# Kernel tuning notes

Hardware: AMD Instinct MI355X
Metric: run time of the kernel (lower is better)

## Reference

```python
import jax, jax.numpy as jnp
import numpy as np

WS = 2        # window size
HEADS = 8
BLOCK = 4     # shuffle block
SCALE = HEADS ** (-0.5)


def conv2d(x, w, groups=1, pad=0):
    return jax.lax.conv_general_dilated(
        x, w, window_strides=(1, 1), padding=[(pad, pad), (pad, pad)],
        dimension_numbers=("NCHW", "OIHW", "NCHW"), feature_group_count=groups)


def shuffle_data(x, block):
    B, C, h, w = x.shape
    x = jnp.transpose(x, (0, 2, 3, 1)).reshape(B, h * w, C)          # b (h w) c
    x = x.reshape(B, block, h // block, block, w // block, C)
    x = jnp.transpose(x, (0, 2, 4, 1, 3, 5)).reshape(B, h * w, C)
    return jnp.transpose(x.reshape(B, h, w, C), (0, 3, 1, 2))         # b c h w


def shuffle_back(x, block):
    B, C, h, w = x.shape
    x = jnp.transpose(x, (0, 2, 3, 1)).reshape(B, h * w, C)
    x = x.reshape(B, h // block, w // block, block, block, C)
    x = jnp.transpose(x, (0, 3, 1, 4, 2, 5)).reshape(B, h * w, C)
    return jnp.transpose(x.reshape(B, h, w, C), (0, 3, 1, 2))


def msa(x):
    # x: [B, C, H, W] with C = 3*dim. NOTE: the original uses a raw reshape
    # (not a permute) to [B, H, W, C]; we replicate that exactly.
    B, C, H, W = x.shape
    x = x.reshape(B, H, W, C)
    hg, wg = H // WS, W // WS
    x = x.reshape(B, hg, WS, wg, WS, C)
    x = jnp.swapaxes(x, 2, 3)                                         # [B,hg,wg,ws,ws,C]
    head_dim = C // 3 // HEADS
    qkv = x.reshape(B, hg * wg, WS * WS, 3, HEADS, head_dim)
    qkv = jnp.transpose(qkv, (3, 0, 1, 4, 2, 5))                      # [3,B,G,h,ws*ws,d]
    q, k, v = qkv[0], qkv[1], qkv[2]
    attn = jnp.einsum("bghqd,bghkd->bghqk", q, k) * SCALE
    attn = jax.nn.softmax(attn, axis=-1)
    out = jnp.einsum("bghqk,bghkd->bghqd", attn, v)
    out = jnp.swapaxes(out, 2, 3).reshape(B, hg, wg, WS, WS, C // 3)
    out = jnp.swapaxes(out, 2, 3)                                     # [B,hg,ws,wg,ws,C/3]
    # raw reshape back to NCHW layout, matching torch .reshape semantics
    return out.reshape(B, C // 3, hg * WS, wg * WS)


def setup_inputs() -> dict:
    key = jax.random.key(0)
    k1, k2, k3, k4 = jax.random.split(key, 4)
    B, dim, H, W = 4, 192, 256, 256
    x = jax.random.normal(k1, (B, dim, H, W), dtype=jnp.float32)
    w_qkv = jax.random.normal(k2, (3 * dim, dim, 1, 1), dtype=jnp.float32) * 0.05
    w_dw = jax.random.normal(k3, (3 * dim, 1, 3, 3), dtype=jnp.float32) * 0.1
    w_proj = jax.random.normal(k4, (dim, dim, 1, 1), dtype=jnp.float32) * 0.05
    return {"x": x, "w_qkv": w_qkv, "w_dw": w_dw, "w_proj": w_proj, "shuffle": 1}


def reference(x, w_qkv, w_dw, w_proj, shuffle):
    if shuffle:
        x = shuffle_data(x, BLOCK)
    qkv = conv2d(conv2d(x, w_qkv), w_dw, groups=w_dw.shape[0], pad=1)
    attn = msa(qkv)
    out = conv2d(attn, w_proj)
    if shuffle:
        out = shuffle_back(out, BLOCK)
    return out
```

## Files before the change

### kernel.cpp

```cpp
#include <hip/hip_runtime.h>
#include <hip/hip_bf16.h>

typedef unsigned short u16;
typedef unsigned int   u32;
typedef __attribute__((ext_vector_type(8))) short s16x8;
typedef __attribute__((ext_vector_type(4))) float f32x4;

__device__ __forceinline__ u16 f2bf(float f) {
  u32 u = __builtin_bit_cast(u32, f);
  return (u16)((u + 0x7FFFu + ((u >> 16) & 1u)) >> 16);
}
__device__ __forceinline__ float bf2f(u16 h) {
  return __builtin_bit_cast(float, (u32)h << 16);
}
__device__ __forceinline__ u32 pack2(float a, float b) {
  __hip_bfloat162 h = __float22bfloat162_rn(make_float2(a, b));
  u32 r;
  __builtin_memcpy(&r, &h, 4);
  return r;
}

__global__ __launch_bounds__(256) void k_wcvt(const float* __restrict__ wq,
                                              const float* __restrict__ wp,
                                              u16* __restrict__ wq_bf,
                                              u16* __restrict__ wp_bf) {
  int i = blockIdx.x * 256 + threadIdx.x;
  if (i < 576 * 192) wq_bf[i] = f2bf(wq[i]);
  if (i < 192 * 192) wp_bf[i] = f2bf(wp[i]);
}

__global__ __launch_bounds__(768, 3) void k_qkv(const float* __restrict__ x,
                                                const u16* __restrict__ wq,
                                                u16* __restrict__ qkv1) {
  __shared__ __align__(16) u16 Xs[256 * 200];
  const int t  = threadIdx.x;
  const int b  = blockIdx.y;
  const int h1 = blockIdx.x;
  const float* xb = x + (size_t)b * 12582912;
  const int hbase = h1 >> 2;
  const int wbase = (h1 & 3) << 4;
#pragma unroll
  for (int it = 0; it < 8; ++it) {
    const int idx = it * 768 + t;
    const int f = idx & 3;
    const int r = (idx >> 2) & 15;
    const int c = (idx >> 6) * 2;
    const int ho = ((r >> 2) & 3) * 64 + hbase;
    const int wo = (r & 3) * 64 + wbase + f * 4;
    const float* s0 = xb + (size_t)c * 65536 + (size_t)ho * 256 + wo;
    float4 v0 = *(const float4*)s0;
    float4 v1 = *(const float4*)(s0 + 65536);
    const int nb = 64 * f + r;
    const int slot = c >> 3;
    const int sl = (slot & 24) | ((slot + 2 * (r & 7)) & 7);
    const int ccol = sl * 8 + (c & 7);
    *(u32*)&Xs[(nb     ) * 200 + ccol] = pack2(v0.x, v1.x);
    *(u32*)&Xs[(nb + 16) * 200 + ccol] = pack2(v0.y, v1.y);
    *(u32*)&Xs[(nb + 32) * 200 + ccol] = pack2(v0.z, v1.z);
    *(u32*)&Xs[(nb + 48) * 200 + ccol] = pack2(v0.w, v1.w);
  }
  __syncthreads();
  const int lane = t & 63, wv = t >> 6;
  const int lm = lane & 15, lk = lane >> 4;
  s16x8 wf[3][6];
#pragma unroll
  for (int mf = 0; mf < 3; ++mf) {
#pragma unroll
    for (int kk = 0; kk < 6; ++kk)
      wf[mf][kk] = *(const s16x8*)&wq[(size_t)(wv * 48 + mf * 16 + lm) * 192 + kk * 32 + lk * 8];
  }
  u16* const ob = qkv1 + (size_t)b * 37748736 + h1 * 256 + lk * 4;
  int slr[6];
#pragma unroll
  for (int kk = 0; kk < 6; ++kk) {
    const int slot = 4 * kk + lk;
    slr[kk] = ((slot & 24) | ((slot + 2 * (lm & 7)) & 7)) * 8;
  }

#pragma unroll 2
  for (int g = 0; g < 16; ++g) {
    s16x8 av[6];
#pragma unroll
    for (int kk = 0; kk < 6; ++kk)
      av[kk] = *(const s16x8*)&Xs[(g * 16 + lm) * 200 + slr[kk]];
    f32x4 acc[3];
#pragma unroll
    for (int mf = 0; mf < 3; ++mf) acc[mf] = f32x4{0.f, 0.f, 0.f, 0.f};
#pragma unroll
    for (int kk = 0; kk < 6; ++kk) {
#pragma unroll
      for (int mf = 0; mf < 3; ++mf)
        acc[mf] = __builtin_amdgcn_mfma_f32_16x16x32_bf16(av[kk], wf[mf][kk], acc[mf], 0, 0, 0);
    }
#pragma unroll
    for (int mf = 0; mf < 3; ++mf) {
      const int ch = wv * 48 + mf * 16 + lm;
      uint2 o;
      o.x = pack2(acc[mf][0], acc[mf][1]);
      o.y = pack2(acc[mf][2], acc[mf][3]);
      *(uint2*)(ob + (size_t)ch * 65536 + g * 16) = o;
    }
  }
}

__global__ __launch_bounds__(512, 2) void k_dwmsa(const u16* __restrict__ qkv1,
                                                  const float* __restrict__ wdw,
                                                  u16* __restrict__ attnb) {
  __shared__ __align__(16) u16 Ds[2][18432];
  const int t = threadIdx.x;
  const int b = blockIdx.y;
  const int gh = blockIdx.x >> 3;
  const int c0 = (blockIdx.x & 7) * 32;
  const u16* qb = qkv1 + (size_t)b * 37748736;

  {
    const int s1 = t >> 8;
    const int tl = t & 255;
    const int lane = t & 63;
    const u32 F = 576u * (u32)((2 * gh + s1) * 256 + c0);
    const int ch0 = (int)(F >> 16);
    const int ch1 = (ch0 < 575) ? ch0 + 1 : 575;
    float wa[9], wb[9];
#pragma unroll
    for (int i = 0; i < 9; ++i) { wa[i] = wdw[ch0 * 9 + i]; wb[i] = wdw[ch1 * 9 + i]; }
#pragma unroll 3
    for (int k = 0; k < 9; ++k) {
      const int ii = (tl + 256 * k) * 8;
      const u32 f = F + (u32)ii;
      const int ch = (int)(f >> 16);
      const int px = (int)(f & 65535u);
      const int h = px >> 8, w0 = px & 255;
      const u16* in = qb + ((size_t)ch << 16);
      const int hm = (h > 0) ? h - 1 : 0;
      const int hp = (h < 255) ? h + 1 : 255;
      uint4 m0 = *(const uint4*)(in + (size_t)hm * 256 + w0);
      uint4 m1 = *(const uint4*)(in + (size_t)h  * 256 + w0);
      uint4 m2 = *(const uint4*)(in + (size_t)hp * 256 + w0);
      u32 p0 = (u32)__shfl((int)m0.w, lane - 1);
      u32 p1 = (u32)__shfl((int)m1.w, lane - 1);
      u32 p2 = (u32)__shfl((int)m2.w, lane - 1);
      u32 n0 = (u32)__shfl((int)m0.x, lane + 1);
      u32 n1 = (u32)__shfl((int)m1.x, lane + 1);
      u32 n2 = (u32)__shfl((int)m2.x, lane + 1);
      const float vm = (h > 0)   ? 1.f : 0.f;
      const float vp = (h < 255) ? 1.f : 0.f;
      const float lmask = (w0 > 0) ? 1.f : 0.f;
      const float rmask = (w0 < 248) ? 1.f : 0.f;
      const bool sec = (ch != ch0);
      float w9[9];
#pragma unroll
      for (int i = 0; i < 9; ++i) w9[i] = sec ? wb[i] : wa[i];
      w9[0] *= vm; w9[1] *= vm; w9[2] *= vm;
      w9[6] *= vp; w9[7] *= vp; w9[8] *= vp;
      float acc[8] = {0.f,0.f,0.f,0.f,0.f,0.f,0.f,0.f};
      const uint4 mids[3] = {m0, m1, m2};
      const u32 prevs[3] = {p0, p1, p2};
      const u32 nexts[3] = {n0, n1, n2};
#pragma unroll
      for (int ky = 0; ky < 3; ++ky) {
        float e[10];
        e[0] = bf2f((u16)(prevs[ky] >> 16)) * lmask;
        u32 uu[4] = {mids[ky].x, mids[ky].y, mids[ky].z, mids[ky].w};
#pragma unroll
        for (int q = 0; q < 4; ++q) {
          e[1 + 2 * q] = bf2f((u16)(uu[q] & 0xffffu));
          e[2 + 2 * q] = bf2f((u16)(uu[q] >> 16));
        }
        e[9] = bf2f((u16)(nexts[ky] & 0xffffu)) * rmask;
#pragma unroll
        for (int kx = 0; kx < 3; ++kx) {
          const float wk = w9[ky * 3 + kx];
#pragma unroll
          for (int jj = 0; jj < 8; ++jj) acc[jj] += wk * e[jj + kx];
        }
      }
      u32 o[4];
#pragma unroll
      for (int q = 0; q < 4; ++q)
        o[q] = pack2(acc[2 * q], acc[2 * q + 1]);
      *(uint4*)&Ds[s1][ii] = make_uint4(o[0], o[1], o[2], o[3]);
    }
  }
  __syncthreads();

  const int lc   = t & 3;
  const int head = (t >> 2) & 7;
  const int win  = t >> 5;
  const int chq  = head * 24 + lc * 6;
  float qv[4][6], kv[4][6], vv[4][6];
#pragma unroll
  for (int s1 = 0; s1 < 2; ++s1) {
#pragma unroll
    for (int s2 = 0; s2 < 2; ++s2) {
      const int tt = s1 * 2 + s2;
      const int base = (2 * win + s2) * 576 + chq;
#pragma unroll
      for (int pp = 0; pp < 3; ++pp) {
        u32 aq = *(const u32*)&Ds[s1][base + 2 * pp];
        u32 ak = *(const u32*)&Ds[s1][base + 192 + 2 * pp];
        u32 av = *(const u32*)&Ds[s1][base + 384 + 2 * pp];
        qv[tt][2 * pp]     = bf2f((u16)(aq & 0xffffu));
        qv[tt][2 * pp + 1] = bf2f((u16)(aq >> 16));
        kv[tt][2 * pp]     = bf2f((u16)(ak & 0xffffu));
        kv[tt][2 * pp + 1] = bf2f((u16)(ak >> 16));
        vv[tt][2 * pp]     = bf2f((u16)(av & 0xffffu));
        vv[tt][2 * pp + 1] = bf2f((u16)(av >> 16));
      }
    }
  }
  float s[4][4];
#pragma unroll
  for (int tq = 0; tq < 4; ++tq) {
#pragma unroll
    for (int tk = 0; tk < 4; ++tk) {
      float d = 0.f;
#pragma unroll
      for (int dd = 0; dd < 6; ++dd) d += qv[tq][dd] * kv[tk][dd];
      d += __shfl_xor(d, 1);
      d += __shfl_xor(d, 2);
      s[tq][tk] = d * 0.35355339059327373f;
    }
  }
  u16* const ab = attnb + (size_t)b * 12582912;
#pragma unroll
  for (int tq = 0; tq < 4; ++tq) {
    float mx = fmaxf(fmaxf(s[tq][0], s[tq][1]), fmaxf(s[tq][2], s[tq][3]));
    float e0 = __expf(s[tq][0] - mx), e1 = __expf(s[tq][1] - mx);
    float e2 = __expf(s[tq][2] - mx), e3 = __expf(s[tq][3] - mx);
    float inv = 1.f / (e0 + e1 + e2 + e3);
    float a0 = e0 * inv, a1 = e1 * inv, a2 = e2 * inv, a3 = e3 * inv;
    float o6[6];
#pragma unroll
    for (int dd = 0; dd < 6; ++dd)
      o6[dd] = a0 * vv[0][dd] + a1 * vv[1][dd] + a2 * vv[2][dd] + a3 * vv[3][dd];
    const int s1 = tq >> 1, s2 = tq & 1;
    const size_t pg = (size_t)((2 * gh + s1) * 256) + c0 + 2 * win + s2;
    u16* dst = ab + pg * 192 + chq;
    *(u32*)(dst)     = pack2(o6[0], o6[1]);
    *(u32*)(dst + 2) = pack2(o6[2], o6[3]);
    *(u32*)(dst + 4) = pack2(o6[4], o6[5]);
  }
}

__global__ __launch_bounds__(512) void k_proj(const u16* __restrict__ attnb,
                                              const u16* __restrict__ wp,
                                              float* __restrict__ out) {
  __shared__ __align__(16) u16 Xs[256 * 200];
  const int t  = threadIdx.x;
  const int b  = blockIdx.y;
  const int hs = blockIdx.x;
  const int pix = t & 255, cg = t >> 8;
  {
    const u16* ab = attnb + (size_t)b * 12582912 + (size_t)hs * 256 + pix;
    u16* xrow = &Xs[pix * 200];
    const int key = (pix >> 4) & 7;
#pragma unroll 8
    for (int i = 0; i < 96; i += 2) {
      const int c = cg * 96 + i;
      const int slot = c >> 3;
      const int sl = (slot & 24) | ((slot + key) & 7);
      u16 v0 = ab[(size_t)c * 65536];
      u16 v1 = ab[(size_t)(c + 1) * 65536];
      *(u32*)&xrow[sl * 8 + (c & 7)] = (u32)v0 | ((u32)v1 << 16);
    }
  }
  __syncthreads();
  const int lane = t & 63, wid = t >> 6;
  const int lm = lane & 15, lk = lane >> 4;
  s16x8 bv[2][6];
#pragma unroll
  for (int rp = 0; rp < 2; ++rp) {
    const int r = 2 * wid + rp;
#pragma unroll
    for (int kk = 0; kk < 6; ++kk) {
      const int slot = 4 * kk + lk;
      const int sl = (slot & 24) | ((slot + (lm & 7)) & 7);
      bv[rp][kk] = *(const s16x8*)&Xs[(16 * lm + r) * 200 + sl * 8];
    }
  }
  float* const ob = out + (size_t)b * 12582912;
  const int hq_base = hs >> 2;
  const int wq_base = (hs & 3) << 4;
  int hqr[2], wq0[2];
#pragma unroll
  for (int rp = 0; rp < 2; ++rp) {
    const int r = 2 * wid + rp;
    hqr[rp] = ((r >> 2) & 3) * 64 + hq_base;
    wq0[rp] = (r & 3) * 64 + wq_base;
  }

#pragma unroll 1
  for (int mt = 0; mt < 3; ++mt) {
    f32x4 acc[4][2];
#pragma unroll
    for (int i = 0; i < 4; ++i) {
      acc[i][0] = f32x4{0.f, 0.f, 0.f, 0.f};
      acc[i][1] = f32x4{0.f, 0.f, 0.f, 0.f};
    }
#pragma unroll
    for (int kk = 0; kk < 6; ++kk) {
      s16x8 af[4];
#pragma unroll
      for (int mf = 0; mf < 4; ++mf)
        af[mf] = *(const s16x8*)&wp[(size_t)(mt * 64 + mf * 16 + lm) * 192 + kk * 32 + lk * 8];
#pragma unroll
      for (int mf = 0; mf < 4; ++mf) {
#pragma unroll
        for (int rp = 0; rp < 2; ++rp)
          acc[mf][rp] = __builtin_amdgcn_mfma_f32_16x16x32_bf16(af[mf], bv[rp][kk], acc[mf][rp], 0, 0, 0);
      }
    }
#pragma unroll
    for (int mf = 0; mf < 4; ++mf) {
#pragma unroll
      for (int rp = 0; rp < 2; ++rp) {
        float* base = ob + (size_t)(mt * 64 + mf * 16 + lk * 4) * 65536
                         + (size_t)hqr[rp] * 256 + wq0[rp] + lm;
#pragma unroll
        for (int rr = 0; rr < 4; ++rr)
          base[(size_t)rr * 65536] = acc[mf][rp][rr];
      }
    }
  }
}

extern "C" void kernel_launch(void* const* d_in, const int* in_sizes, int n_in,
                              void* d_out, int out_size, void* d_ws, size_t ws_size,
                              hipStream_t stream) {
  const float* x   = (const float*)d_in[0];
  const float* wq  = (const float*)d_in[1];
  const float* wdw = (const float*)d_in[2];
  const float* wpr = (const float*)d_in[3];
  float* out = (float*)d_out;
  u16* ws = (u16*)d_ws;
  u16* wq_bf = ws;
  u16* wp_bf = ws + 110592;
  u16* qkv1  = ws + 147456;
  u16* attnb = qkv1 + (size_t)150994944;

  hipLaunchKernelGGL(k_wcvt,  dim3(432), dim3(256), 0, stream, wq, wpr, wq_bf, wp_bf);
  hipLaunchKernelGGL(k_qkv,   dim3(256, 4), dim3(768), 0, stream, x, wq_bf, qkv1);
  hipLaunchKernelGGL(k_dwmsa, dim3(1024, 4), dim3(512), 0, stream, qkv1, wdw, attnb);
  hipLaunchKernelGGL(k_proj,  dim3(256, 4), dim3(512), 0, stream, attnb, wp_bf, out);
}
```

Before: 397.5 us.

## Split QKV input staging in two halves to overlap loads with MFMA

The k_qkv kernel now stages only the first half of the pixel tile into shared memory before computing. It issues global loads for the second half into registers, runs MFMAs on the first 8 row groups, then writes the second half to LDS and finishes. The aim is to hide global-load latency behind compute. It adds 32 float registers per thread and an extra barrier, which may lower occupancy under the 768-thread, 3-blocks-per-SM launch bound.

```diff
diff --git a/kernel.cpp b/kernel.cpp
--- a/kernel.cpp
+++ b/kernel.cpp
@@ -40,11 +40,11 @@
   const int hbase = h1 >> 2;
   const int wbase = (h1 & 3) << 4;
 #pragma unroll
-  for (int it = 0; it < 8; ++it) {
+  for (int it = 0; it < 4; ++it) {
     const int idx = it * 768 + t;
-    const int f = idx & 3;
-    const int r = (idx >> 2) & 15;
-    const int c = (idx >> 6) * 2;
+    const int f = idx & 1;
+    const int r = (idx >> 1) & 15;
+    const int c = (idx >> 5) * 2;
     const int ho = ((r >> 2) & 3) * 64 + hbase;
     const int wo = (r & 3) * 64 + wbase + f * 4;
     const float* s0 = xb + (size_t)c * 65536 + (size_t)ho * 256 + wo;
@@ -60,6 +60,19 @@
     *(u32*)&Xs[(nb + 48) * 200 + ccol] = pack2(v0.w, v1.w);
   }
   __syncthreads();
+  float4 vb0[4], vb1[4];
+#pragma unroll
+  for (int it = 0; it < 4; ++it) {
+    const int idx = it * 768 + t;
+    const int f = idx & 1;
+    const int r = (idx >> 1) & 15;
+    const int c = (idx >> 5) * 2;
+    const int ho = ((r >> 2) & 3) * 64 + hbase;
+    const int wo = (r & 3) * 64 + wbase + 8 + f * 4;
+    const float* s0 = xb + (size_t)c * 65536 + (size_t)ho * 256 + wo;
+    vb0[it] = *(const float4*)s0;
+    vb1[it] = *(const float4*)(s0 + 65536);
+  }
   const int lane = t & 63, wv = t >> 6;
   const int lm = lane & 15, lk = lane >> 4;
   s16x8 wf[3][6];
@@ -78,7 +91,47 @@
   }
 
 #pragma unroll 2
-  for (int g = 0; g < 16; ++g) {
+  for (int g = 0; g < 8; ++g) {
+    s16x8 av[6];
+#pragma unroll
+    for (int kk = 0; kk < 6; ++kk)
+      av[kk] = *(const s16x8*)&Xs[(g * 16 + lm) * 200 + slr[kk]];
+    f32x4 acc[3];
+#pragma unroll
+    for (int mf = 0; mf < 3; ++mf) acc[mf] = f32x4{0.f, 0.f, 0.f, 0.f};
+#pragma unroll
+    for (int kk = 0; kk < 6; ++kk) {
+#pragma unroll
+      for (int mf = 0; mf < 3; ++mf)
+        acc[mf] = __builtin_amdgcn_mfma_f32_16x16x32_bf16(av[kk], wf[mf][kk], acc[mf], 0, 0, 0);
+    }
+#pragma unroll
+    for (int mf = 0; mf < 3; ++mf) {
+      const int ch = wv * 48 + mf * 16 + lm;
+      uint2 o;
+      o.x = pack2(acc[mf][0], acc[mf][1]);
+      o.y = pack2(acc[mf][2], acc[mf][3]);
+      *(uint2*)(ob + (size_t)ch * 65536 + g * 16) = o;
+    }
+  }
+#pragma unroll
+  for (int it = 0; it < 4; ++it) {
+    const int idx = it * 768 + t;
+    const int f = idx & 1;
+    const int r = (idx >> 1) & 15;
+    const int c = (idx >> 5) * 2;
+    const int nb = 128 + 64 * f + r;
+    const int slot = c >> 3;
+    const int sl = (slot & 24) | ((slot + 2 * (r & 7)) & 7);
+    const int ccol = sl * 8 + (c & 7);
+    *(u32*)&Xs[(nb     ) * 200 + ccol] = pack2(vb0[it].x, vb1[it].x);
+    *(u32*)&Xs[(nb + 16) * 200 + ccol] = pack2(vb0[it].y, vb1[it].y);
+    *(u32*)&Xs[(nb + 32) * 200 + ccol] = pack2(vb0[it].z, vb1[it].z);
+    *(u32*)&Xs[(nb + 48) * 200 + ccol] = pack2(vb0[it].w, vb1[it].w);
+  }
+  __syncthreads();
+#pragma unroll 2
+  for (int g = 8; g < 16; ++g) {
     s16x8 av[6];
 #pragma unroll
     for (int kk = 0; kk < 6; ++kk)
```

Result: slower. 440.1 us (+10.7%).
